# Optimization experiments

Hardware: AMD Instinct MI355X
Metric: run time of the kernel (lower is better)

Reference implementation:

```python
import jax, jax.numpy as jnp
import numpy as np
from jax import lax

D_MODEL = 768
N_LAYERS = 2
D_STATE = 16
D_CONV = 4
EXPAND = 2
D_INNER = EXPAND * D_MODEL
DT_RANK = 48  # ceil(768/16)
BETA = 0.9
ALPHA = 1.0
NS_STEPS = 1
EPS = 1e-5
BATCH = 2
SEQ = 512


def rmsnorm(x, w):
    return x * lax.rsqrt(jnp.mean(x * x, axis=-1, keepdims=True) + EPS) * w


def newton_schulz(X, steps):
    # Muon quintic Newton-Schulz orthogonalization on (B, D_INNER, D_STATE) matrices.
    a, b, c = 3.4445, -4.7750, 2.0315
    G = jnp.swapaxes(X, -1, -2)  # (B, N, Di) rows < cols
    G = G / (jnp.sqrt(jnp.sum(G * G, axis=(-2, -1), keepdims=True)) + 1e-7)
    for _ in range(steps):
        A = G @ jnp.swapaxes(G, -1, -2)  # (B, N, N)
        G = a * G + (b * A + c * (A @ A)) @ G
    return jnp.swapaxes(G, -1, -2)


def mamba_mixer(x, in_w, cw, cb, xp_w, dtp_w, dtp_b, A_log, Dp, out_w):
    B_, L, _ = x.shape
    xz = jnp.einsum('bld,ed->ble', x, in_w)  # (B, L, 2*Di)
    xi, z = jnp.split(xz, 2, axis=-1)
    # causal depthwise conv1d + silu
    xc = lax.conv_general_dilated(
        jnp.swapaxes(xi, 1, 2), cw, window_strides=(1,),
        padding=[(D_CONV - 1, 0)],
        dimension_numbers=('NCH', 'OIH', 'NCH'),
        feature_group_count=D_INNER)
    xc = jax.nn.silu(jnp.swapaxes(xc, 1, 2) + cb)  # (B, L, Di)
    x_dbl = jnp.einsum('bld,ed->ble', xc, xp_w)
    dt_lr = x_dbl[..., :DT_RANK]
    Bm = x_dbl[..., DT_RANK:DT_RANK + D_STATE]  # (B, L, N)
    Cm = x_dbl[..., DT_RANK + D_STATE:]         # (B, L, N)
    dt = jax.nn.softplus(jnp.einsum('blr,dr->bld', dt_lr, dtp_w) + dtp_b)
    A = -jnp.exp(A_log)  # (Di, N)
    dA = jnp.exp(dt[..., None] * A)                            # (B, L, Di, N)
    dBx = dt[..., None] * Bm[:, :, None, :] * xc[..., None]    # (B, L, Di, N)

    def step(carry, inp):
        h, v = carry
        dA_t, dBx_t, C_t = inp
        v = BETA * v + dBx_t                 # momentum velocity
        vu = newton_schulz(v, NS_STEPS)      # NS-orthogonalized update
        h = dA_t * h + ALPHA * vu
        y = jnp.einsum('bdn,bn->bd', h, C_t)
        return (h, v), y

    h0 = jnp.zeros((B_, D_INNER, D_STATE), x.dtype)
    v0 = jnp.zeros_like(h0)
    xs = (jnp.moveaxis(dA, 1, 0), jnp.moveaxis(dBx, 1, 0), jnp.moveaxis(Cm, 1, 0))
    _, ys = lax.scan(step, (h0, v0), xs)
    y = jnp.moveaxis(ys, 0, 1) + Dp * xc
    y = y * jax.nn.silu(z)
    return jnp.einsum('bld,ed->ble', y, out_w)


def forward(x, in_proj_w, conv_w, conv_b, x_proj_w, dt_proj_w, dt_proj_b,
            A_log, D, out_proj_w, norm_w, final_norm_w):
    for i in range(N_LAYERS):
        x = mamba_mixer(rmsnorm(x, norm_w[i]), in_proj_w[i], conv_w[i], conv_b[i],
                        x_proj_w[i], dt_proj_w[i], dt_proj_b[i], A_log[i], D[i],
                        out_proj_w[i]) + x
    return rmsnorm(x, final_norm_w)


def setup_inputs() -> dict:
    key = jax.random.key(0)
    ks = jax.random.split(key, 8)
    s = 0.02
    scale_out = s / np.sqrt(2 * N_LAYERS)
    A_init = jnp.broadcast_to(jnp.arange(1, D_STATE + 1, dtype=jnp.float32), (N_LAYERS, D_INNER, D_STATE))
    return {
        'x': jax.random.normal(ks[0], (BATCH, SEQ, D_MODEL), jnp.float32),
        'in_proj_w': jax.random.normal(ks[1], (N_LAYERS, 2 * D_INNER, D_MODEL), jnp.float32) * s,
        'conv_w': jax.random.normal(ks[2], (N_LAYERS, D_INNER, 1, D_CONV), jnp.float32) * 0.5,
        'conv_b': jnp.zeros((N_LAYERS, D_INNER), jnp.float32),
        'x_proj_w': jax.random.normal(ks[3], (N_LAYERS, DT_RANK + 2 * D_STATE, D_INNER), jnp.float32) * s,
        'dt_proj_w': jax.random.normal(ks[4], (N_LAYERS, D_INNER, DT_RANK), jnp.float32) * (DT_RANK ** -0.5),
        'dt_proj_b': jax.random.uniform(ks[5], (N_LAYERS, D_INNER), jnp.float32, -4.0, -2.0),
        'A_log': jnp.log(A_init),
        'D': jnp.ones((N_LAYERS, D_INNER), jnp.float32),
        'out_proj_w': jax.random.normal(ks[6], (N_LAYERS, D_MODEL, D_INNER), jnp.float32) * scale_out,
        'norm_w': jnp.ones((N_LAYERS, D_MODEL), jnp.float32),
        'final_norm_w': jnp.ones((D_MODEL,), jnp.float32),
    }


def reference(x, in_proj_w, conv_w, conv_b, x_proj_w, dt_proj_w, dt_proj_b,
              A_log, D, out_proj_w, norm_w, final_norm_w):
    return forward(x, in_proj_w, conv_w, conv_b, x_proj_w, dt_proj_w, dt_proj_b,
                   A_log, D, out_proj_w, norm_w, final_norm_w)
```

## Files before the change

kernel.cpp:

```cpp
#include <hip/hip_runtime.h>
#include <math.h>

#define DM   768
#define DI   1536
#define NDS  16
#define DTR  48
#define XDC  80
#define XPN  128
#define NB   2
#define SEQL 512
#define NT   (NB*SEQL)
#define CC   64
#define TT   8
#define BETA 0.9f
#define NSA  3.4445f
#define NSB  (-4.775f)
#define NSC  2.0315f
#define LOG2E 1.4426950408889634f
#define GKH  768
#define GKS  772

typedef __attribute__((ext_vector_type(8))) short short8v;
typedef __attribute__((ext_vector_type(4))) float f32x4;

__device__ __forceinline__ float silu_(float x){ return x / (1.f + __expf(-x)); }
__device__ __forceinline__ unsigned short bfr(float x){
  unsigned u = __float_as_uint(x);
  return (unsigned short)((u + 0x7fffu + ((u>>16)&1u)) >> 16);
}
__device__ __forceinline__ void gl_lds16(const unsigned short* g, unsigned short* l){
  __builtin_amdgcn_global_load_lds((const __attribute__((address_space(1))) void*)g,
                                   (__attribute__((address_space(3))) void*)l, 16, 0, 0);
}

__global__ void rms_k(const float* __restrict__ X, const float* __restrict__ W,
                      unsigned short* __restrict__ O)
{
  const int g = blockIdx.x, tid = threadIdx.x;
  const float* xr = X + (size_t)g*DM;
  float x0 = xr[tid], x1 = xr[tid+256], x2 = xr[tid+512];
  float ss = x0*x0 + x1*x1 + x2*x2;
  #pragma unroll
  for (int m=1; m<=32; m<<=1) ss += __shfl_xor(ss, m);
  __shared__ float ws[4];
  if ((tid & 63) == 0) ws[tid>>6] = ss;
  __syncthreads();
  float sc = rsqrtf((ws[0]+ws[1]+ws[2]+ws[3])*(1.f/DM) + 1e-5f);
  unsigned short* o = O + (size_t)g*DM;
  o[tid]     = bfr(x0*sc*W[tid]);
  o[tid+256] = bfr(x1*sc*W[tid+256]);
  o[tid+512] = bfr(x2*sc*W[tid+512]);
}

__global__ void castbf_k(const float* __restrict__ in, unsigned short* __restrict__ out, int n4)
{
  const int i = blockIdx.x*256 + threadIdx.x;
  if (i >= n4) return;
  float4 v = ((const float4*)in)[i];
  ushort4 o;
  o.x = bfr(v.x); o.y = bfr(v.y); o.z = bfr(v.z); o.w = bfr(v.w);
  ((ushort4*)out)[i] = o;
}

__global__ void castpad_k(const float* __restrict__ in, unsigned short* __restrict__ out)
{
  const int i = blockIdx.x*256 + threadIdx.x;
  const int total = 2*XPN*DI/4;
  if (i >= total) return;
  const int l = i / (XPN*DI/4);
  const int r = i % (XPN*DI/4);
  const int row = r / (DI/4);
  const int k4 = r % (DI/4);
  ushort4 o = {0,0,0,0};
  if (row < XDC){
    float4 v = *(const float4*)(in + ((size_t)l*XDC + row)*DI + k4*4);
    o.x = bfr(v.x); o.y = bfr(v.y); o.z = bfr(v.z); o.w = bfr(v.w);
  }
  ((ushort4*)out)[i] = o;
}

__global__ __launch_bounds__(256) void gemm_mf(
    const unsigned short* __restrict__ Abf, int lda,
    const unsigned short* __restrict__ Bbf, int ldb,
    float* __restrict__ Out, float* __restrict__ Part,
    int M, int N, int K, int SK)
{
  __shared__ unsigned short As[128*32];
  __shared__ unsigned short Bs[128*32];
  const int tid  = threadIdx.x;
  const int wid  = tid >> 6, lane = tid & 63;
  const int bm   = blockIdx.y*128, bn = blockIdx.x*128;
  const int kc   = K/SK, kBeg = blockIdx.z*kc, kEnd = kBeg + kc;
  const int wr   = (wid>>1)*64, wc = (wid&1)*64;

  f32x4 acc[4][4];
  #pragma unroll
  for (int m=0;m<4;m++)
    #pragma unroll
    for (int n=0;n<4;n++) acc[m][n] = (f32x4){0.f,0.f,0.f,0.f};

  const int e0 = (wid*2)*512 + lane*8;
  const int e1 = e0 + 512;
  const int r0 = e0 >> 5, k0e = e0 & 31;
  const int r1 = e1 >> 5, k1e = e1 & 31;
  const unsigned short* Ag0 = Abf + (size_t)(bm + r0)*lda + k0e;
  const unsigned short* Ag1 = Abf + (size_t)(bm + r1)*lda + k1e;
  const unsigned short* Bg0 = Bbf + (size_t)(bn + r0)*ldb + k0e;
  const unsigned short* Bg1 = Bbf + (size_t)(bn + r1)*ldb + k1e;

  int aoff[4], boff[4];
  #pragma unroll
  for (int m=0;m<4;m++) aoff[m] = (wr + m*16 + (lane&15))*32 + (lane>>4)*8;
  #pragma unroll
  for (int n=0;n<4;n++) boff[n] = (wc + n*16 + (lane&15))*32 + (lane>>4)*8;

  for (int k0 = kBeg; k0 < kEnd; k0 += 32){
    gl_lds16(Ag0 + k0, As + e0);
    gl_lds16(Ag1 + k0, As + e1);
    gl_lds16(Bg0 + k0, Bs + e0);
    gl_lds16(Bg1 + k0, Bs + e1);
    __syncthreads();
    short8v af[4], bfv[4];
    #pragma unroll
    for (int m=0;m<4;m++) af[m]  = *(const short8v*)(As + aoff[m]);
    #pragma unroll
    for (int n=0;n<4;n++) bfv[n] = *(const short8v*)(Bs + boff[n]);
    #pragma unroll
    for (int m=0;m<4;m++)
      #pragma unroll
      for (int n=0;n<4;n++)
        acc[m][n] = __builtin_amdgcn_mfma_f32_16x16x32_bf16(af[m], bfv[n], acc[m][n], 0, 0, 0);
    __syncthreads();
  }

  #pragma unroll
  for (int m=0;m<4;m++){
    const int rowb = bm + wr + m*16 + (lane>>4)*4;
    #pragma unroll
    for (int n=0;n<4;n++){
      const int col = bn + wc + n*16 + (lane&15);
      #pragma unroll
      for (int r=0;r<4;r++){
        const int row = rowb + r;
        if (SK == 1) Out[(size_t)row*N + col] = acc[m][n][r];
        else         Part[(size_t)blockIdx.z*M*N + (size_t)row*N + col] = acc[m][n][r];
      }
    }
  }
}

__global__ void gemm64w(const float* __restrict__ A, int lda,
                        const float* __restrict__ Bw, int ldb,
                        float* __restrict__ Out, float* __restrict__ wOut,
                        const float* __restrict__ bias, const float* __restrict__ xc,
                        int M, int N, int K)
{
  __shared__ float As[16][64], Bs[16][64];
  const int tid = threadIdx.x;
  const int bm = blockIdx.y*64, bn = blockIdx.x*64;
  const int lr = tid>>2, lk = (tid&3)<<2;
  const int tx = tid&15, ty = tid>>4;
  float acc[4][4];
  #pragma unroll
  for (int i=0;i<4;i++)
    #pragma unroll
    for (int j=0;j<4;j++) acc[i][j] = 0.f;
  const float* Ap = A + (size_t)(bm+lr)*lda + lk;
  const float* Bp = Bw + (size_t)(bn+lr)*ldb + lk;
  for (int k0=0; k0<K; k0+=16){
    float4 a0 = *(const float4*)(Ap + k0);
    float4 b0 = *(const float4*)(Bp + k0);
    __syncthreads();
    As[lk+0][lr]=a0.x; As[lk+1][lr]=a0.y; As[lk+2][lr]=a0.z; As[lk+3][lr]=a0.w;
    Bs[lk+0][lr]=b0.x; Bs[lk+1][lr]=b0.y; Bs[lk+2][lr]=b0.z; Bs[lk+3][lr]=b0.w;
    __syncthreads();
    #pragma unroll
    for (int kk=0;kk<16;kk++){
      float a[4], b[4];
      *(float4*)a = *(const float4*)&As[kk][ty*4];
      *(float4*)b = *(const float4*)&Bs[kk][tx*4];
      #pragma unroll
      for (int i=0;i<4;i++)
        #pragma unroll
        for (int j=0;j<4;j++) acc[i][j] = fmaf(a[i], b[j], acc[i][j]);
    }
  }
  #pragma unroll
  for (int i=0;i<4;i++){
    const int row = bm + ty*4 + i;
    #pragma unroll
    for (int j=0;j<4;j++){
      const int col = bn + tx*4 + j;
      float vv = acc[i][j] + bias[col];
      vv = fmaxf(vv,0.f) + log1pf(__expf(-fabsf(vv)));
      Out[(size_t)row*N+col]  = vv;
      wOut[(size_t)row*N+col] = vv * xc[(size_t)row*N+col];
    }
  }
}

__global__ void reducepad_k(const float* __restrict__ Part, float* __restrict__ Out)
{
  const int i = blockIdx.x*256 + threadIdx.x;
  if (i >= NT*XDC) return;
  const int row = i / XDC, col = i % XDC;
  float s = 0.f;
  #pragma unroll
  for (int z=0; z<8; z++) s += Part[(size_t)z*NT*XPN + (size_t)row*XPN + col];
  Out[i] = s;
}

template<int MODE>
__global__ void reduce_rms_k(const float* __restrict__ Part, const float* __restrict__ res,
                             const float* __restrict__ W, float* __restrict__ nxt,
                             unsigned short* __restrict__ xnb, float* __restrict__ dout)
{
  const int g = blockIdx.x, tid = threadIdx.x;
  float s[3];
  #pragma unroll
  for (int j=0;j<3;j++){
    const int e = tid + j*256;
    float v = res[(size_t)g*DM + e];
    #pragma unroll
    for (int z=0;z<4;z++) v += Part[(size_t)z*NT*DM + (size_t)g*DM + e];
    s[j] = v;
    if (MODE==1) nxt[(size_t)g*DM + e] = v;
  }
  float ss = s[0]*s[0] + s[1]*s[1] + s[2]*s[2];
  #pragma unroll
  for (int m=1; m<=32; m<<=1) ss += __shfl_xor(ss, m);
  __shared__ float ws[4];
  if ((tid & 63) == 0) ws[tid>>6] = ss;
  __syncthreads();
  float sc = rsqrtf((ws[0]+ws[1]+ws[2]+ws[3])*(1.f/DM) + 1e-5f);
  #pragma unroll
  for (int j=0;j<3;j++){
    const int e = tid + j*256;
    if (MODE==1) xnb[(size_t)g*DM + e] = bfr(s[j]*sc*W[e]);
    else         dout[(size_t)g*DM + e] = s[j]*sc*W[e];
  }
}

__global__ void conv_k(const float* __restrict__ xz, const float* __restrict__ cw,
                       const float* __restrict__ cb, float* __restrict__ xc,
                       unsigned short* __restrict__ xc16)
{
  const int d = blockIdx.x*256 + threadIdx.x;
  const int g = blockIdx.y;
  const int b = g >> 9, t = g & (SEQL-1);
  float4 w4 = *(const float4*)(cw + (size_t)d*4);
  const float wk[4] = {w4.x, w4.y, w4.z, w4.w};
  const float* col = xz + ((size_t)b*SEQL)*(2*DI) + d;
  float acc = cb[d];
  #pragma unroll
  for (int k=0;k<4;k++){
    int tt = t - 3 + k;
    if (tt >= 0) acc = fmaf(wk[k], col[(size_t)tt*(2*DI)], acc);
  }
  const float r = silu_(acc);
  xc[(size_t)g*DI + d]   = r;
  xc16[(size_t)g*DI + d] = bfr(r);
}

__global__ void vagg_k(const float* __restrict__ dt, const float* __restrict__ wb,
                       const float* __restrict__ xdbl, float* __restrict__ Vagg,
                       float* __restrict__ S, float* __restrict__ cumdt)
{
  const int d = blockIdx.x*256 + threadIdx.x;
  const int c = blockIdx.y, b = blockIdx.z;
  float acc[16];
  #pragma unroll
  for (int n=0;n<16;n++) acc[n] = 0.f;
  float sdt = 0.f;
  for (int s=0;s<TT;s++){
    const int g = b*SEQL + c*TT + s;
    sdt += dt[(size_t)g*DI + d];
    cumdt[(size_t)g*DI + d] = sdt;
    const float w = wb[(size_t)g*DI + d];
    #pragma unroll
    for (int n=0;n<16;n++) acc[n] = fmaf(BETA, acc[n], w * xdbl[(size_t)g*XDC + 48 + n]);
  }
  const size_t base = ((size_t)(b*CC + c)*NDS)*DI + d;
  #pragma unroll
  for (int n=0;n<16;n++) Vagg[base + (size_t)n*DI] = acc[n];
  S[(size_t)(b*CC + c)*DI + d] = sdt;
}

__global__ void vcomb_k(float* V, float betaT)
{
  const int d = blockIdx.x*256 + threadIdx.x;
  const int n = blockIdx.y, b = blockIdx.z;
  const size_t stride = (size_t)NDS*DI;
  size_t idx = ((size_t)(b*CC)*NDS + n)*DI + d;
  float v = 0.f;
  for (int c=0;c<CC;c++){
    const float a = V[idx];
    V[idx] = v;
    v = fmaf(betaT, v, a);
    idx += stride;
  }
}

__global__ __launch_bounds__(256) void gram_k(
    const float* __restrict__ vst, const float* __restrict__ wb,
    const float* __restrict__ xdbl, float* __restrict__ Qg)
{
  const int c = blockIdx.x, b = blockIdx.y;
  const int tid = threadIdx.x;
  __shared__ float Xs[24*GKS];
  __shared__ float Ms[24][25];
  __shared__ float sB[8][16];
  __shared__ float Rm[16][17];

  const size_t vbase = ((size_t)(b*CC + c)*NDS)*DI;
  const size_t gbase = (size_t)(b*SEQL + c*TT);

  const bool active = tid < 252;
  const int tile = tid / 12, seg = tid % 12;
  int ti = 0, tj = 0;
  {
    int tt = tile;
    if (active){ while (tt >= 6 - ti){ tt -= 6 - ti; ti++; } tj = ti + tt; }
  }
  const int i0 = ti*4, j0 = tj*4;
  const int ks = seg*64;
  float acc[4][4];
  #pragma unroll
  for (int i=0;i<4;i++)
    #pragma unroll
    for (int j=0;j<4;j++) acc[i][j] = 0.f;

  for (int pass = 0; pass < 2; pass++){
    const int koff = pass * GKH;
    __syncthreads();
    #pragma unroll
    for (int q = 0; q < 18; q++){
      const int p = tid + q*256;
      const int col = p / 192;
      const int kk  = (p % 192) * 4;
      float4 xv;
      if (col < 16) xv = *(const float4*)(vst + vbase + (size_t)col*DI + koff + kk);
      else          xv = *(const float4*)(wb + (gbase + (col-16))*DI + koff + kk);
      *(float4*)(Xs + col*GKS + kk) = xv;
    }
    __syncthreads();
    if (active){
      for (int k4 = 0; k4 < 64; k4 += 4){
        float4 av[4], bv[4];
        #pragma unroll
        for (int r=0;r<4;r++) av[r] = *(const float4*)(Xs + (i0+r)*GKS + ks + k4);
        #pragma unroll
        for (int r=0;r<4;r++) bv[r] = *(const float4*)(Xs + (j0+r)*GKS + ks + k4);
        #pragma unroll
        for (int i=0;i<4;i++)
          #pragma unroll
          for (int j=0;j<4;j++){
            float s = fmaf(av[i].x, bv[j].x, acc[i][j]);
            s = fmaf(av[i].y, bv[j].y, s);
            s = fmaf(av[i].z, bv[j].z, s);
            acc[i][j] = fmaf(av[i].w, bv[j].w, s);
          }
      }
    }
  }
  __syncthreads();
  if (active){
    #pragma unroll
    for (int e=0;e<16;e++) Xs[(tile*16 + e)*12 + seg] = acc[e>>2][e&3];
  }
  if (tid < 128){ const int s = tid>>4, n = tid&15; sB[s][n] = xdbl[(gbase + s)*XDC + 48 + n]; }
  __syncthreads();
  for (int o = tid; o < 336; o += 256){
    const int tl = o >> 4, e = o & 15;
    int tt = tl, ti2 = 0;
    while (tt >= 6 - ti2){ tt -= 6 - ti2; ti2++; }
    const int tj2 = ti2 + tt;
    const int i = ti2*4 + (e>>2), j = tj2*4 + (e&3);
    float s = 0.f;
    #pragma unroll
    for (int sg=0; sg<12; sg++) s += Xs[o*12 + sg];
    Ms[i][j] = s; Ms[j][i] = s;
  }
  __syncthreads();

  const int i = tid >> 4, j = tid & 15;
  float Rreg = Ms[i][j];
  constexpr float PB[9] = {1.f, 0.9f, 0.81f, 0.729f, 0.6561f, 0.59049f,
                           0.531441f, 0.4782969f, 0.43046721f};
  const size_t qbase = ((size_t)(b*CC + c)*TT)*256;
  #pragma unroll
  for (int t=0;t<TT;t++){
    float p_i = PB[t]*Ms[i][16+t];
    float p_j = PB[t]*Ms[j][16+t];
    #pragma unroll
    for (int r=0;r<t;r++){
      const float gg = Ms[16+r][16+t];
      p_i = fmaf(PB[t-1-r]*gg, sB[r][i], p_i);
      p_j = fmaf(PB[t-1-r]*gg, sB[r][j], p_j);
    }
    const float bi = sB[t][i], bj = sB[t][j];
    const float gtt = Ms[16+t][16+t];
    Rreg = BETA*BETA*Rreg + BETA*(p_i*bj + bi*p_j) + gtt*bi*bj;
    Rm[i][j] = Rreg;
    __syncthreads();
    float tr = 0.f;
    #pragma unroll
    for (int k=0;k<16;k++) tr += Rm[k][k];
    const float nu = sqrtf(tr) + 1e-7f;
    const float inv_nu = 1.f/nu;
    const float inv2 = inv_nu*inv_nu;
    const float inv4 = inv2*inv2;
    float a2v = 0.f;
    #pragma unroll
    for (int k=0;k<16;k++) a2v = fmaf(Rm[i][k], Rm[k][j], a2v);
    float q = NSB*inv2*Rreg + NSC*inv4*a2v;
    if (i == j) q += NSA;
    Qg[qbase + t*256 + tid] = q * inv_nu;
    __syncthreads();
  }
}

__global__ __launch_bounds__(256) void apply_k(
    float* vh, const float* __restrict__ dt,
    const float* __restrict__ wb, const float* __restrict__ xdbl,
    const float* __restrict__ Qg, const float* __restrict__ A_log,
    float* __restrict__ ylocal)
{
  const int c = blockIdx.x, b = blockIdx.y, z = blockIdx.z;
  const int tid = threadIdx.x;
  const int d = z*256 + tid;
  __shared__ float sQ[8*256];
  __shared__ float sBC[8][32];

  const size_t qbase = ((size_t)(b*CC + c)*TT)*256;
  #pragma unroll
  for (int q=0;q<8;q++) sQ[q*256 + tid] = Qg[qbase + q*256 + tid];
  {
    const int s = tid >> 5, idx = tid & 31;
    sBC[s][idx] = xdbl[(size_t)(b*SEQL + c*TT + s)*XDC + 48 + idx];
  }
  __syncthreads();

  float v[16], h[16], Ar[16];
  {
    float* vs = vh + ((size_t)(b*CC + c)*NDS)*DI + d;
    const float* arow = A_log + (size_t)d*NDS;
    #pragma unroll
    for (int n=0;n<16;n++){
      v[n] = vs[(size_t)n*DI];
      h[n] = 0.f;
      Ar[n] = -__expf(arow[n]) * LOG2E;
    }
  }

  for (int t=0;t<TT;t++){
    const size_t g = (size_t)(b*SEQL + c*TT + t);
    const float dtv = dt[g*DI + d];
    const float wv  = wb[g*DI + d];
    #pragma unroll
    for (int n=0;n<16;n++) v[n] = fmaf(BETA, v[n], wv*sBC[t][n]);
    float un[16];
    #pragma unroll
    for (int n=0;n<16;n++) un[n] = 0.f;
    const float* qt = sQ + t*256;
    #pragma unroll
    for (int k=0;k<16;k++){
      const float vk = v[k];
      const float4 q0 = *(const float4*)(qt + k*16);
      const float4 q1 = *(const float4*)(qt + k*16 + 4);
      const float4 q2 = *(const float4*)(qt + k*16 + 8);
      const float4 q3 = *(const float4*)(qt + k*16 + 12);
      un[0]=fmaf(vk,q0.x,un[0]); un[1]=fmaf(vk,q0.y,un[1]); un[2]=fmaf(vk,q0.z,un[2]); un[3]=fmaf(vk,q0.w,un[3]);
      un[4]=fmaf(vk,q1.x,un[4]); un[5]=fmaf(vk,q1.y,un[5]); un[6]=fmaf(vk,q1.z,un[6]); un[7]=fmaf(vk,q1.w,un[7]);
      un[8]=fmaf(vk,q2.x,un[8]); un[9]=fmaf(vk,q2.y,un[9]); un[10]=fmaf(vk,q2.z,un[10]); un[11]=fmaf(vk,q2.w,un[11]);
      un[12]=fmaf(vk,q3.x,un[12]); un[13]=fmaf(vk,q3.y,un[13]); un[14]=fmaf(vk,q3.z,un[14]); un[15]=fmaf(vk,q3.w,un[15]);
    }
    float y = 0.f;
    #pragma unroll
    for (int n=0;n<16;n++){
      const float e = exp2f(dtv*Ar[n]);
      h[n] = fmaf(e, h[n], un[n]);
      y = fmaf(h[n], sBC[t][16+n], y);
    }
    ylocal[g*DI + d] = y;
  }
  float* he = vh + ((size_t)(b*CC + c)*NDS)*DI + d;
  #pragma unroll
  for (int n=0;n<16;n++) he[(size_t)n*DI] = h[n];
}

__global__ void hcomb_k(float* H, const float* __restrict__ S,
                        const float* __restrict__ A_log)
{
  const int d = blockIdx.x*256 + threadIdx.x;
  const int n = blockIdx.y, b = blockIdx.z;
  const float An = -__expf(A_log[(size_t)d*NDS + n]);
  const size_t stride = (size_t)NDS*DI;
  size_t idx  = ((size_t)(b*CC)*NDS + n)*DI + d;
  size_t sidx = (size_t)(b*CC)*DI + d;
  float hv = 0.f;
  for (int c=0;c<CC;c++){
    const float a = H[idx];
    H[idx] = hv;
    hv = fmaf(__expf(An * S[sidx]), hv, a);
    idx += stride; sidx += DI;
  }
}

__global__ void yepi_k(const float* __restrict__ ylocal, const float* __restrict__ hst,
                       const float* __restrict__ cumdt, const float* __restrict__ xdbl,
                       const float* __restrict__ A_log, const float* __restrict__ Dv,
                       const float* __restrict__ xcp, const float* __restrict__ xz,
                       unsigned short* __restrict__ ybf)
{
  const int d = blockIdx.x*256 + threadIdx.x;
  const int g = blockIdx.y;
  const int b = g >> 9, t = g & (SEQL-1);
  const int c = t / TT;
  const float ddt = cumdt[(size_t)g*DI + d];
  const float* hs = hst + ((size_t)(b*CC + c)*NDS)*DI + d;
  const float* ar = A_log + (size_t)d*NDS;
  float corr = 0.f;
  #pragma unroll
  for (int n=0;n<16;n++){
    float An = -__expf(ar[n]);
    float Cn = xdbl[(size_t)g*XDC + 64 + n];
    corr = fmaf(hs[(size_t)n*DI] * __expf(An*ddt), Cn, corr);
  }
  float y = ylocal[(size_t)g*DI + d] + corr + Dv[d]*xcp[(size_t)g*DI + d];
  float z = xz[(size_t)g*(2*DI) + DI + d];
  ybf[(size_t)g*DI + d] = bfr(y * silu_(z));
}

extern "C" void kernel_launch(void* const* d_in, const int* in_sizes, int n_in,
                              void* d_out, int out_size, void* d_ws, size_t ws_size,
                              hipStream_t stream)
{
  (void)in_sizes; (void)n_in; (void)out_size; (void)ws_size;
  const float* x      = (const float*)d_in[0];
  const float* in_w   = (const float*)d_in[1];
  const float* conv_w = (const float*)d_in[2];
  const float* conv_b = (const float*)d_in[3];
  const float* xp_w   = (const float*)d_in[4];
  const float* dtp_w  = (const float*)d_in[5];
  const float* dtp_b  = (const float*)d_in[6];
  const float* A_log  = (const float*)d_in[7];
  const float* Dp     = (const float*)d_in[8];
  const float* out_w  = (const float*)d_in[9];
  const float* norm_w = (const float*)d_in[10];
  const float* fnorm  = (const float*)d_in[11];

  const float betaT = powf(BETA, (float)TT);

  float* w0 = (float*)d_ws; size_t off = 0;
  auto alloc = [&](size_t n)->float*{ float* p = w0 + off; off += (n + 63) & ~(size_t)63; return p; };
  float* xa     = alloc((size_t)NT*DM);
  float* bfA    = alloc((size_t)NT*DI/2);
  float* xz     = alloc((size_t)NT*2*DI);
  float* xcb    = alloc((size_t)NT*DI);
  float* xcbbF  = alloc((size_t)NT*DI/2);
  float* xdbl   = alloc((size_t)NT*XDC);
  float* dtb    = alloc((size_t)NT*DI);
  float* wbuf   = alloc((size_t)NT*DI);
  float* cumdt  = alloc((size_t)NT*DI);
  float* ylocal = alloc((size_t)NT*DI);
  float* Sbuf   = alloc((size_t)NB*CC*DI);
  float* Qg     = alloc((size_t)NB*CC*TT*256);
  float* big1   = alloc((size_t)NB*CC*NDS*DI);
  float* wInF   = alloc((size_t)2*2*DI*DM/2);
  float* wOutF  = alloc((size_t)2*DM*DI/2);
  float* wXpF   = alloc((size_t)2*XPN*DI/2);

  unsigned short* xnb  = (unsigned short*)bfA;
  unsigned short* ybf  = (unsigned short*)bfA;
  unsigned short* xcbb = (unsigned short*)xcbbF;
  unsigned short* wInb = (unsigned short*)wInF;
  unsigned short* wOutb= (unsigned short*)wOutF;
  unsigned short* wXpb = (unsigned short*)wXpF;
  float* partb = big1;

  castbf_k<<<dim3((2*2*DI*DM/4+255)/256), dim3(256), 0, stream>>>(in_w, wInb, 2*2*DI*DM/4);
  castbf_k<<<dim3((2*DM*DI/4+255)/256), dim3(256), 0, stream>>>(out_w, wOutb, 2*DM*DI/4);
  castpad_k<<<dim3((2*XPN*DI/4+255)/256), dim3(256), 0, stream>>>(xp_w, wXpb);
  rms_k<<<dim3(NT), dim3(256), 0, stream>>>(x, norm_w, xnb);

  const float* xcur = x;
  for (int l=0; l<2; l++){
    const unsigned short* wIn_l  = wInb  + (size_t)l*2*DI*DM;
    const unsigned short* wOut_l = wOutb + (size_t)l*DM*DI;
    const unsigned short* wXp_l  = wXpb  + (size_t)l*XPN*DI;
    const float* cw_l  = conv_w + (size_t)l*DI*4;
    const float* cb_l  = conv_b + (size_t)l*DI;
    const float* dtw_l = dtp_w  + (size_t)l*DI*DTR;
    const float* dtbi  = dtp_b  + (size_t)l*DI;
    const float* al_l  = A_log  + (size_t)l*DI*NDS;
    const float* d_l   = Dp     + (size_t)l*DI;

    gemm_mf<<<dim3(2*DI/128, NT/128, 1), dim3(256), 0, stream>>>(
        xnb, DM, wIn_l, DM, xz, nullptr, NT, 2*DI, DM, 1);
    conv_k<<<dim3(DI/256, NT), dim3(256), 0, stream>>>(xz, cw_l, cb_l, xcb, xcbb);
    gemm_mf<<<dim3(XPN/128, NT/128, 8), dim3(256), 0, stream>>>(
        xcbb, DI, wXp_l, DI, nullptr, partb, NT, XPN, DI, 8);
    reducepad_k<<<dim3((NT*XDC+255)/256), dim3(256), 0, stream>>>(partb, xdbl);
    gemm64w<<<dim3(DI/64, NT/64, 1), dim3(256), 0, stream>>>(
        xdbl, XDC, dtw_l, DTR, dtb, wbuf, dtbi, xcb, NT, DI, DTR);
    vagg_k<<<dim3(DI/256, CC, NB), dim3(256), 0, stream>>>(dtb, wbuf, xdbl, big1, Sbuf, cumdt);
    vcomb_k<<<dim3(DI/256, NDS, NB), dim3(256), 0, stream>>>(big1, betaT);
    gram_k<<<dim3(CC, NB), dim3(256), 0, stream>>>(big1, wbuf, xdbl, Qg);
    apply_k<<<dim3(CC, NB, DI/256), dim3(256), 0, stream>>>(
        big1, dtb, wbuf, xdbl, Qg, al_l, ylocal);
    hcomb_k<<<dim3(DI/256, NDS, NB), dim3(256), 0, stream>>>(big1, Sbuf, al_l);
    yepi_k<<<dim3(DI/256, NT), dim3(256), 0, stream>>>(
        ylocal, big1, cumdt, xdbl, al_l, d_l, xcb, xz, ybf);
    gemm_mf<<<dim3(DM/128, NT/128, 4), dim3(256), 0, stream>>>(
        ybf, DI, wOut_l, DI, nullptr, partb, NT, DM, DI, 4);
    if (l == 0)
      reduce_rms_k<1><<<dim3(NT), dim3(256), 0, stream>>>(
          partb, xcur, norm_w + DM, xa, xnb, nullptr);
    else
      reduce_rms_k<2><<<dim3(NT), dim3(256), 0, stream>>>(
          partb, xcur, fnorm, nullptr, nullptr, (float*)d_out);
    xcur = xa;
  }
}
```

Measured before the change: 423.4 us.

## Double chunk length to 16 steps and fuse weight casts into one kernel

Changes the chunked momentum/NS scan from 64 chunks of 8 steps to 32 chunks of 16 steps and widens the Gram kernel to handle 32 columns with a 8x8 tile triangle. Sequential combine kernels (vcomb, hcomb) become shorter chains with software-prefetched next loads, and the per-chunk dt sum is read from cumdt instead of a separate buffer. The three weight-cast kernels are merged into one launch, and GEMM split-K partials get a dedicated buffer instead of aliasing big1. Larger chunks shift work into the Gram/apply kernels and cut the parallelism of per-chunk grids.

```diff
diff --git a/kernel.cpp b/kernel.cpp
--- a/kernel.cpp
+++ b/kernel.cpp
@@ -10,8 +10,8 @@
 #define NB   2
 #define SEQL 512
 #define NT   (NB*SEQL)
-#define CC   64
-#define TT   8
+#define CC   32
+#define TT   16
 #define BETA 0.9f
 #define NSA  3.4445f
 #define NSB  (-4.775f)
@@ -19,6 +19,7 @@
 #define LOG2E 1.4426950408889634f
 #define GKH  768
 #define GKS  772
+#define NCOL 32
 
 typedef __attribute__((ext_vector_type(8))) short short8v;
 typedef __attribute__((ext_vector_type(4))) float f32x4;
@@ -52,31 +53,39 @@
   o[tid+512] = bfr(x2*sc*W[tid+512]);
 }
 
-__global__ void castbf_k(const float* __restrict__ in, unsigned short* __restrict__ out, int n4)
-{
-  const int i = blockIdx.x*256 + threadIdx.x;
-  if (i >= n4) return;
-  float4 v = ((const float4*)in)[i];
-  ushort4 o;
-  o.x = bfr(v.x); o.y = bfr(v.y); o.z = bfr(v.z); o.w = bfr(v.w);
-  ((ushort4*)out)[i] = o;
-}
-
-__global__ void castpad_k(const float* __restrict__ in, unsigned short* __restrict__ out)
-{
-  const int i = blockIdx.x*256 + threadIdx.x;
-  const int total = 2*XPN*DI/4;
-  if (i >= total) return;
-  const int l = i / (XPN*DI/4);
-  const int r = i % (XPN*DI/4);
-  const int row = r / (DI/4);
-  const int k4 = r % (DI/4);
-  ushort4 o = {0,0,0,0};
-  if (row < XDC){
-    float4 v = *(const float4*)(in + ((size_t)l*XDC + row)*DI + k4*4);
-    o.x = bfr(v.x); o.y = bfr(v.y); o.z = bfr(v.z); o.w = bfr(v.w);
-  }
-  ((ushort4*)out)[i] = o;
+__global__ void castall_k(const float* __restrict__ in_w, const float* __restrict__ out_w,
+                          const float* __restrict__ xp_w,
+                          unsigned short* __restrict__ wIn, unsigned short* __restrict__ wOut,
+                          unsigned short* __restrict__ wXp)
+{
+  const int T0 = 2*2*DI*DM/4, T1 = 2*DM*DI/4, T2 = 2*XPN*DI/4;
+  int i = blockIdx.x*256 + threadIdx.x;
+  if (i < T0){
+    float4 v = ((const float4*)in_w)[i];
+    ushort4 o = { bfr(v.x), bfr(v.y), bfr(v.z), bfr(v.w) };
+    ((ushort4*)wIn)[i] = o;
+    return;
+  }
+  i -= T0;
+  if (i < T1){
+    float4 v = ((const float4*)out_w)[i];
+    ushort4 o = { bfr(v.x), bfr(v.y), bfr(v.z), bfr(v.w) };
+    ((ushort4*)wOut)[i] = o;
+    return;
+  }
+  i -= T1;
+  if (i < T2){
+    const int l = i / (XPN*DI/4);
+    const int r = i % (XPN*DI/4);
+    const int row = r / (DI/4);
+    const int k4 = r % (DI/4);
+    ushort4 o = {0,0,0,0};
+    if (row < XDC){
+      float4 v = *(const float4*)(xp_w + ((size_t)l*XDC + row)*DI + k4*4);
+      o.x = bfr(v.x); o.y = bfr(v.y); o.z = bfr(v.z); o.w = bfr(v.w);
+    }
+    ((ushort4*)wXp)[i] = o;
+  }
 }
 
 __global__ __launch_bounds__(256) void gemm_mf(
@@ -264,7 +273,7 @@
 
 __global__ void vagg_k(const float* __restrict__ dt, const float* __restrict__ wb,
                        const float* __restrict__ xdbl, float* __restrict__ Vagg,
-                       float* __restrict__ S, float* __restrict__ cumdt)
+                       float* __restrict__ cumdt)
 {
   const int d = blockIdx.x*256 + threadIdx.x;
   const int c = blockIdx.y, b = blockIdx.z;
@@ -283,7 +292,6 @@
   const size_t base = ((size_t)(b*CC + c)*NDS)*DI + d;
   #pragma unroll
   for (int n=0;n<16;n++) Vagg[base + (size_t)n*DI] = acc[n];
-  S[(size_t)(b*CC + c)*DI + d] = sdt;
 }
 
 __global__ void vcomb_k(float* V, float betaT)
@@ -292,12 +300,13 @@
   const int n = blockIdx.y, b = blockIdx.z;
   const size_t stride = (size_t)NDS*DI;
   size_t idx = ((size_t)(b*CC)*NDS + n)*DI + d;
+  float a = V[idx];
   float v = 0.f;
   for (int c=0;c<CC;c++){
-    const float a = V[idx];
+    float an = (c+1<CC) ? V[idx+stride] : 0.f;
     V[idx] = v;
     v = fmaf(betaT, v, a);
-    idx += stride;
+    a = an; idx += stride;
   }
 }
 
@@ -307,23 +316,23 @@
 {
   const int c = blockIdx.x, b = blockIdx.y;
   const int tid = threadIdx.x;
-  __shared__ float Xs[24*GKS];
-  __shared__ float Ms[24][25];
-  __shared__ float sB[8][16];
+  __shared__ float Xs[NCOL*GKS];
+  __shared__ float Ms[NCOL][NCOL+1];
+  __shared__ float sB[TT][16];
   __shared__ float Rm[16][17];
 
   const size_t vbase = ((size_t)(b*CC + c)*NDS)*DI;
   const size_t gbase = (size_t)(b*SEQL + c*TT);
 
-  const bool active = tid < 252;
-  const int tile = tid / 12, seg = tid % 12;
+  const bool active = tid < 216;
+  const int tile = tid / 6, seg = tid % 6;
   int ti = 0, tj = 0;
   {
     int tt = tile;
-    if (active){ while (tt >= 6 - ti){ tt -= 6 - ti; ti++; } tj = ti + tt; }
+    if (active){ while (tt >= 8 - ti){ tt -= 8 - ti; ti++; } tj = ti + tt; }
   }
   const int i0 = ti*4, j0 = tj*4;
-  const int ks = seg*64;
+  const int ks = seg*128;
   float acc[4][4];
   #pragma unroll
   for (int i=0;i<4;i++)
@@ -334,7 +343,7 @@
     const int koff = pass * GKH;
     __syncthreads();
     #pragma unroll
-    for (int q = 0; q < 18; q++){
+    for (int q = 0; q < 24; q++){
       const int p = tid + q*256;
       const int col = p / 192;
       const int kk  = (p % 192) * 4;
@@ -345,7 +354,7 @@
     }
     __syncthreads();
     if (active){
-      for (int k4 = 0; k4 < 64; k4 += 4){
+      for (int k4 = 0; k4 < 128; k4 += 4){
         float4 av[4], bv[4];
         #pragma unroll
         for (int r=0;r<4;r++) av[r] = *(const float4*)(Xs + (i0+r)*GKS + ks + k4);
@@ -366,27 +375,30 @@
   __syncthreads();
   if (active){
     #pragma unroll
-    for (int e=0;e<16;e++) Xs[(tile*16 + e)*12 + seg] = acc[e>>2][e&3];
-  }
-  if (tid < 128){ const int s = tid>>4, n = tid&15; sB[s][n] = xdbl[(gbase + s)*XDC + 48 + n]; }
+    for (int e=0;e<16;e++) Xs[(tile*16 + e)*6 + seg] = acc[e>>2][e&3];
+  }
+  { const int s = tid>>4, n = tid&15; sB[s][n] = xdbl[(gbase + s)*XDC + 48 + n]; }
   __syncthreads();
-  for (int o = tid; o < 336; o += 256){
+  for (int o = tid; o < 576; o += 256){
     const int tl = o >> 4, e = o & 15;
     int tt = tl, ti2 = 0;
-    while (tt >= 6 - ti2){ tt -= 6 - ti2; ti2++; }
+    while (tt >= 8 - ti2){ tt -= 8 - ti2; ti2++; }
     const int tj2 = ti2 + tt;
     const int i = ti2*4 + (e>>2), j = tj2*4 + (e&3);
     float s = 0.f;
     #pragma unroll
-    for (int sg=0; sg<12; sg++) s += Xs[o*12 + sg];
+    for (int sg=0; sg<6; sg++) s += Xs[o*6 + sg];
     Ms[i][j] = s; Ms[j][i] = s;
   }
   __syncthreads();
 
   const int i = tid >> 4, j = tid & 15;
   float Rreg = Ms[i][j];
-  constexpr float PB[9] = {1.f, 0.9f, 0.81f, 0.729f, 0.6561f, 0.59049f,
-                           0.531441f, 0.4782969f, 0.43046721f};
+  constexpr float PB[17] = {1.f, 0.9f, 0.81f, 0.729f, 0.6561f, 0.59049f,
+                            0.531441f, 0.4782969f, 0.43046721f, 0.387420489f,
+                            0.3486784401f, 0.31381059609f, 0.282429536481f,
+                            0.2541865828329f, 0.22876792454961f, 0.205891132094649f,
+                            0.1853020188851841f};
   const size_t qbase = ((size_t)(b*CC + c)*TT)*256;
   #pragma unroll
   for (int t=0;t<TT;t++){
@@ -429,15 +441,16 @@
   const int c = blockIdx.x, b = blockIdx.y, z = blockIdx.z;
   const int tid = threadIdx.x;
   const int d = z*256 + tid;
-  __shared__ float sQ[8*256];
-  __shared__ float sBC[8][32];
+  __shared__ float sQ[TT*256];
+  __shared__ float sBC[TT][32];
 
   const size_t qbase = ((size_t)(b*CC + c)*TT)*256;
   #pragma unroll
-  for (int q=0;q<8;q++) sQ[q*256 + tid] = Qg[qbase + q*256 + tid];
-  {
-    const int s = tid >> 5, idx = tid & 31;
-    sBC[s][idx] = xdbl[(size_t)(b*SEQL + c*TT + s)*XDC + 48 + idx];
+  for (int q=0;q<TT;q++) sQ[q*256 + tid] = Qg[qbase + q*256 + tid];
+  #pragma unroll
+  for (int rr=0; rr<2; rr++){
+    const int p = tid + rr*256;
+    sBC[p>>5][p&31] = xdbl[(size_t)((size_t)b*SEQL + c*TT + (p>>5))*XDC + 48 + (p&31)];
   }
   __syncthreads();
 
@@ -489,21 +502,26 @@
   for (int n=0;n<16;n++) he[(size_t)n*DI] = h[n];
 }
 
-__global__ void hcomb_k(float* H, const float* __restrict__ S,
+__global__ void hcomb_k(float* H, const float* __restrict__ cumdt,
                         const float* __restrict__ A_log)
 {
   const int d = blockIdx.x*256 + threadIdx.x;
   const int n = blockIdx.y, b = blockIdx.z;
   const float An = -__expf(A_log[(size_t)d*NDS + n]);
   const size_t stride = (size_t)NDS*DI;
+  const size_t sstep = (size_t)TT*DI;
   size_t idx  = ((size_t)(b*CC)*NDS + n)*DI + d;
-  size_t sidx = (size_t)(b*CC)*DI + d;
+  size_t sidx = ((size_t)b*SEQL + TT-1)*DI + d;
+  float a = H[idx];
+  float sv = cumdt[sidx];
   float hv = 0.f;
   for (int c=0;c<CC;c++){
-    const float a = H[idx];
+    float an = 0.f, sn = 0.f;
+    if (c+1 < CC){ an = H[idx+stride]; sn = cumdt[sidx+sstep]; }
     H[idx] = hv;
-    hv = fmaf(__expf(An * S[sidx]), hv, a);
-    idx += stride; sidx += DI;
+    hv = fmaf(__expf(An * sv), hv, a);
+    a = an; sv = sn;
+    idx += stride; sidx += sstep;
   }
 }
 
@@ -564,9 +582,9 @@
   float* wbuf   = alloc((size_t)NT*DI);
   float* cumdt  = alloc((size_t)NT*DI);
   float* ylocal = alloc((size_t)NT*DI);
-  float* Sbuf   = alloc((size_t)NB*CC*DI);
   float* Qg     = alloc((size_t)NB*CC*TT*256);
   float* big1   = alloc((size_t)NB*CC*NDS*DI);
+  float* partb  = alloc((size_t)4*NT*DM);
   float* wInF   = alloc((size_t)2*2*DI*DM/2);
   float* wOutF  = alloc((size_t)2*DM*DI/2);
   float* wXpF   = alloc((size_t)2*XPN*DI/2);
@@ -577,11 +595,12 @@
   unsigned short* wInb = (unsigned short*)wInF;
   unsigned short* wOutb= (unsigned short*)wOutF;
   unsigned short* wXpb = (unsigned short*)wXpF;
-  float* partb = big1;
-
-  castbf_k<<<dim3((2*2*DI*DM/4+255)/256), dim3(256), 0, stream>>>(in_w, wInb, 2*2*DI*DM/4);
-  castbf_k<<<dim3((2*DM*DI/4+255)/256), dim3(256), 0, stream>>>(out_w, wOutb, 2*DM*DI/4);
-  castpad_k<<<dim3((2*XPN*DI/4+255)/256), dim3(256), 0, stream>>>(xp_w, wXpb);
+
+  {
+    const int T0 = 2*2*DI*DM/4, T1 = 2*DM*DI/4, T2 = 2*XPN*DI/4;
+    castall_k<<<dim3((T0+T1+T2+255)/256), dim3(256), 0, stream>>>(
+        in_w, out_w, xp_w, wInb, wOutb, wXpb);
+  }
   rms_k<<<dim3(NT), dim3(256), 0, stream>>>(x, norm_w, xnb);
 
   const float* xcur = x;
@@ -604,12 +623,12 @@
     reducepad_k<<<dim3((NT*XDC+255)/256), dim3(256), 0, stream>>>(partb, xdbl);
     gemm64w<<<dim3(DI/64, NT/64, 1), dim3(256), 0, stream>>>(
         xdbl, XDC, dtw_l, DTR, dtb, wbuf, dtbi, xcb, NT, DI, DTR);
-    vagg_k<<<dim3(DI/256, CC, NB), dim3(256), 0, stream>>>(dtb, wbuf, xdbl, big1, Sbuf, cumdt);
+    vagg_k<<<dim3(DI/256, CC, NB), dim3(256), 0, stream>>>(dtb, wbuf, xdbl, big1, cumdt);
     vcomb_k<<<dim3(DI/256, NDS, NB), dim3(256), 0, stream>>>(big1, betaT);
     gram_k<<<dim3(CC, NB), dim3(256), 0, stream>>>(big1, wbuf, xdbl, Qg);
     apply_k<<<dim3(CC, NB, DI/256), dim3(256), 0, stream>>>(
         big1, dtb, wbuf, xdbl, Qg, al_l, ylocal);
-    hcomb_k<<<dim3(DI/256, NDS, NB), dim3(256), 0, stream>>>(big1, Sbuf, al_l);
+    hcomb_k<<<dim3(DI/256, NDS, NB), dim3(256), 0, stream>>>(big1, cumdt, al_l);
     yepi_k<<<dim3(DI/256, NT), dim3(256), 0, stream>>>(
         ylocal, big1, cumdt, xdbl, al_l, d_l, xcb, xz, ybf);
     gemm_mf<<<dim3(DM/128, NT/128, 4), dim3(256), 0, stream>>>(
```

Result: slower. 441.9 us (+4.4%).
